# Kernel tuning notes

Hardware: AMD Instinct MI355X
Metric: run time of the kernel (lower is better)

The kernel has to match this reference:

```python
import jax, jax.numpy as jnp
import numpy as np

B, N, DIN, DOUT = 8, 2048, 128, 128

def setup_inputs() -> dict:
    key = jax.random.key(0)
    k1, k2, k3, k4 = jax.random.split(key, 4)
    x = jax.random.normal(k1, (B, N, DIN), dtype=jnp.float32)
    adj = jax.random.uniform(k2, (B, N, N), dtype=jnp.float32)
    W = jax.random.normal(k3, (DIN, DOUT), dtype=jnp.float32) / np.sqrt(DIN)
    b = jax.random.normal(k4, (DOUT,), dtype=jnp.float32) * 0.01
    return {"x": x, "adj": adj, "W": W, "b": b}

def reference(x, adj, W, b):
    # degree over last dim of adj: [B, N]
    degree = jnp.sum(adj, axis=2)
    d_norm = 1.0 / jnp.sqrt(degree + 1e-8)
    # D^{-1/2} A D^{-1/2} == row/col elementwise scaling (same math as diag_embed+bmm)
    adj_norm = d_norm[:, :, None] * adj * d_norm[:, None, :]
    support = jnp.einsum('bnm,bmd->bnd', adj_norm, x)  # [B, N, DIN]
    return support @ W + b  # [B, N, DOUT]
```

## Files before the change

### kernel.cpp

```cpp
#include <hip/hip_runtime.h>
#include <hip/hip_bf16.h>

#define NN 2048
#define DD 128

typedef __attribute__((ext_vector_type(4))) float f32x4;
typedef __attribute__((ext_vector_type(8))) short short8;
typedef __attribute__((ext_vector_type(2))) unsigned int u32x2;

__device__ __forceinline__ unsigned short f2bf_bits(float f) {
  union { __hip_bfloat16 h; unsigned short s; } u;
  u.h = __float2bfloat16(f);
  return u.s;
}

__device__ __forceinline__ short8 cvt8(f32x4 a, f32x4 b) {
  short8 r;
  r[0] = (short)f2bf_bits(a[0]); r[1] = (short)f2bf_bits(a[1]);
  r[2] = (short)f2bf_bits(a[2]); r[3] = (short)f2bf_bits(a[3]);
  r[4] = (short)f2bf_bits(b[0]); r[5] = (short)f2bf_bits(b[1]);
  r[6] = (short)f2bf_bits(b[2]); r[7] = (short)f2bf_bits(b[3]);
  return r;
}

__global__ void k_degree(const float* __restrict__ adj, float* __restrict__ dnorm) {
  const int wv = threadIdx.x >> 6;
  const int ln = threadIdx.x & 63;
  const int row = blockIdx.x * 4 + wv;
  const f32x4* rowp = (const f32x4*)(adj + (size_t)row * NN);
  float s = 0.0f;
#pragma unroll
  for (int i = 0; i < 8; ++i) {
    f32x4 v = rowp[i * 64 + ln];
    s += v[0] + v[1] + v[2] + v[3];
  }
#pragma unroll
  for (int off = 32; off >= 1; off >>= 1) s += __shfl_xor(s, off);
  if (ln == 0) dnorm[row] = rsqrtf(s + 1e-8f);
}

__global__ void k_y(const float* __restrict__ x, const float* __restrict__ W,
                    const float* __restrict__ dnorm, short* __restrict__ yT) {
  const int ln = threadIdx.x & 63;
  const int wv = threadIdx.x >> 6;
  const int bb = blockIdx.x >> 5;
  const int n0 = (blockIdx.x & 31) << 6;
  const int l15 = ln & 15, l4 = ln >> 4;
  const int dbase = wv * 32;

  short8 af[2][4];
#pragma unroll
  for (int dt = 0; dt < 2; ++dt)
#pragma unroll
    for (int ks = 0; ks < 4; ++ks) {
      short8 a;
#pragma unroll
      for (int j = 0; j < 8; ++j)
        a[j] = (short)f2bf_bits(W[(size_t)(ks * 32 + l4 * 8 + j) * DD + dbase + dt * 16 + l15]);
      af[dt][ks] = a;
    }

  f32x4 acc[2][4];
#pragma unroll
  for (int dt = 0; dt < 2; ++dt)
#pragma unroll
    for (int nt = 0; nt < 4; ++nt) acc[dt][nt] = (f32x4)0.0f;

  const float* xb = x + (size_t)bb * NN * DD;
  const float* dnb = dnorm + (size_t)bb * NN;
#pragma unroll
  for (int nt = 0; nt < 4; ++nt) {
    const int n = n0 + nt * 16 + l15;
    const float dn = dnb[n];
#pragma unroll
    for (int ks = 0; ks < 4; ++ks) {
      f32x4 p = *(const f32x4*)(xb + (size_t)n * DD + ks * 32 + l4 * 8);
      f32x4 q = *(const f32x4*)(xb + (size_t)n * DD + ks * 32 + l4 * 8 + 4);
      short8 bf = cvt8(p * dn, q * dn);
#pragma unroll
      for (int dt = 0; dt < 2; ++dt)
        acc[dt][nt] = __builtin_amdgcn_mfma_f32_16x16x32_bf16(af[dt][ks], bf, acc[dt][nt], 0, 0, 0);
    }
  }

  short* yb = yT + (size_t)bb * DD * NN;
#pragma unroll
  for (int dt = 0; dt < 2; ++dt)
#pragma unroll
    for (int nt = 0; nt < 4; ++nt)
#pragma unroll
      for (int r = 0; r < 4; ++r) {
        int d = dbase + dt * 16 + l4 * 4 + r;
        yb[(size_t)d * NN + n0 + nt * 16 + l15] = (short)f2bf_bits(acc[dt][nt][r]);
      }
}

__launch_bounds__(512, 4)
__global__ void k_gemm(const float* __restrict__ adj, const short* __restrict__ yT,
                       const float* __restrict__ dnorm, const float* __restrict__ bias,
                       float* __restrict__ out) {
  __shared__ short As[4][2048];

  const int t = threadIdx.x;
  const int ln = t & 63;
  const int wv = t >> 6;
  const int orig = ((blockIdx.x & 7) << 6) | (blockIdx.x >> 3);
  const int bb = orig >> 6;
  const int m0 = (orig & 63) << 5;

  const float* ablk = adj + ((size_t)bb * NN + m0) * NN;
  const int oc = (wv << 4) + (ln & 15);
  const int kg8 = (ln >> 4) << 3;
  const short* ybase = yT + ((size_t)bb * DD + oc) * NN;

  const unsigned srow = (unsigned)t >> 4;
  const unsigned sc4 = ((unsigned)t & 15u) << 2;

  f32x4 acc[2];
  acc[0] = (f32x4)0.0f; acc[1] = (f32x4)0.0f;

  auto loadA = [&](int tile) -> f32x4 {
    return *(const f32x4*)(ablk + (size_t)srow * NN + ((tile & 31) << 6) + sc4);
  };
  auto loadB = [&](int tile, int ks) -> short8 {
    return *(const short8*)(ybase + ((tile & 31) << 6) + ks * 32 + kg8);
  };
  auto writeA = [&](f32x4 v, int buf) {
    unsigned byte = (srow << 7) + (sc4 << 1);
    byte ^= (srow & 7u) << 4;
    u32x2 u;
    u[0] = (unsigned)f2bf_bits(v[0]) | ((unsigned)f2bf_bits(v[1]) << 16);
    u[1] = (unsigned)f2bf_bits(v[2]) | ((unsigned)f2bf_bits(v[3]) << 16);
    *(u32x2*)((char*)As + (buf << 12) + byte) = u;
  };
  auto compute = [&](int buf, short8 b0, short8 b1) {
    const char* base = (const char*)As + (buf << 12);
#pragma unroll
    for (int ks = 0; ks < 2; ++ks) {
      short8 bf = ks ? b1 : b0;
#pragma unroll
      for (int m = 0; m < 2; ++m) {
        unsigned row = (unsigned)(m * 16 + (ln & 15));
        unsigned byte = (row << 7) + (unsigned)((ks * 32 + kg8) << 1);
        byte ^= (row & 7u) << 4;
        short8 a = *(const short8*)(base + byte);
        acc[m] = __builtin_amdgcn_mfma_f32_16x16x32_bf16(a, bf, acc[m], 0, 0, 0);
      }
    }
  };

  f32x4 sA0 = loadA(0), sA1 = loadA(1), sA2 = loadA(2), sA3 = loadA(3);
  short8 bE0 = loadB(0, 0), bE1 = loadB(0, 1);
  short8 bO0 = loadB(1, 0), bO1 = loadB(1, 1);
  writeA(sA0, 0);
  asm volatile("s_waitcnt lgkmcnt(0)\n\ts_barrier" ::: "memory");

#define GITER(T, SNEW, SWR, BC0, BC1)                                 \
  {                                                                   \
    SNEW = loadA((T) + 4);                                            \
    short8 nb0 = loadB((T) + 2, 0), nb1 = loadB((T) + 2, 1);          \
    writeA(SWR, ((T) + 1) & 3);                                       \
    asm volatile("s_waitcnt lgkmcnt(0)\n\ts_barrier" ::: "memory");   \
    compute((T) & 3, BC0, BC1);                                       \
    BC0 = nb0; BC1 = nb1;                                             \
  }

#pragma unroll 1
  for (int t4 = 0; t4 < 32; t4 += 4) {
    GITER(t4 + 0, sA0, sA1, bE0, bE1);
    GITER(t4 + 1, sA1, sA2, bO0, bO1);
    GITER(t4 + 2, sA2, sA3, bE0, bE1);
    GITER(t4 + 3, sA3, sA0, bO0, bO1);
  }
#undef GITER

  const float bv = bias[oc];
  const int rbase = (ln >> 4) << 2;
#pragma unroll
  for (int m = 0; m < 2; ++m) {
    f32x4 dn = *(const f32x4*)(dnorm + (size_t)bb * NN + m0 + m * 16 + rbase);
#pragma unroll
    for (int r = 0; r < 4; ++r)
      out[(size_t)(bb * NN + m0 + m * 16 + rbase + r) * DD + oc] = acc[m][r] * dn[r] + bv;
  }
}

extern "C" void kernel_launch(void* const* d_in, const int* in_sizes, int n_in,
                              void* d_out, int out_size, void* d_ws, size_t ws_size,
                              hipStream_t stream) {
  (void)in_sizes; (void)n_in; (void)out_size; (void)ws_size;
  const float* x = (const float*)d_in[0];
  const float* adj = (const float*)d_in[1];
  const float* W = (const float*)d_in[2];
  const float* bias = (const float*)d_in[3];
  float* out = (float*)d_out;

  char* ws = (char*)d_ws;
  float* dnorm = (float*)ws;
  short* yT = (short*)(ws + (1 << 16));

  k_degree<<<4096, 256, 0, stream>>>(adj, dnorm);
  k_y<<<256, 256, 0, stream>>>(x, W, dnorm, yT);
  k_gemm<<<512, 512, 0, stream>>>(adj, yT, dnorm, bias, out);
}
```

Measured before the change: 69.25 us.

## Fuse degree, projection and aggregation into one cooperative kernel reading adj once

```diff
diff --git a/kernel.cpp b/kernel.cpp
--- a/kernel.cpp
+++ b/kernel.cpp
@@ -1,8 +1,11 @@
 #include <hip/hip_runtime.h>
 #include <hip/hip_bf16.h>
+#include <hip/hip_cooperative_groups.h>
 
 #define NN 2048
 #define DD 128
+
+namespace cg = cooperative_groups;
 
 typedef __attribute__((ext_vector_type(4))) float f32x4;
 typedef __attribute__((ext_vector_type(8))) short short8;
@@ -21,6 +24,161 @@
   r[4] = (short)f2bf_bits(b[0]); r[5] = (short)f2bf_bits(b[1]);
   r[6] = (short)f2bf_bits(b[2]); r[7] = (short)f2bf_bits(b[3]);
   return r;
+}
+
+__device__ __forceinline__ u32x2 pack4(f32x4 v) {
+  u32x2 u;
+  u[0] = (unsigned)f2bf_bits(v[0]) | ((unsigned)f2bf_bits(v[1]) << 16);
+  u[1] = (unsigned)f2bf_bits(v[2]) | ((unsigned)f2bf_bits(v[3]) << 16);
+  return u;
+}
+
+#define ABIG_S 1032
+#define DBUF_S 72
+__launch_bounds__(512, 2)
+__global__ void k_fused(const float* __restrict__ adj, const float* __restrict__ x,
+                        const float* __restrict__ W, const float* __restrict__ bias,
+                        float* __restrict__ out, short* __restrict__ yT) {
+  __shared__ short Abig[64 * ABIG_S];
+  __shared__ short dbuf[2][64 * DBUF_S];
+  __shared__ float dnl[64];
+
+  const int t = threadIdx.x;
+  const int ln = t & 63;
+  const int wv = t >> 6;
+  const int l15 = ln & 15, l4 = ln >> 4;
+
+  const int orig = ((blockIdx.x & 7) << 5) | (blockIdx.x >> 3);
+  const int bb = orig >> 5;
+  const int rowblk = orig & 31;
+  const size_t rowg0 = (size_t)bb * NN + (rowblk << 6);
+
+  const int r = t >> 3, c8 = t & 7;
+  const float* arow = adj + (rowg0 + r) * NN + (c8 << 2);
+  char* awr = (char*)Abig + r * (ABIG_S * 2) + (c8 << 3);
+
+  float s0 = 0.f, s1 = 0.f;
+  u32x2 areg[32];
+#pragma unroll
+  for (int T = 0; T < 32; ++T) {
+    f32x4 v = *(const f32x4*)(arow + T * 32);
+    s0 += v[0] + v[1]; s1 += v[2] + v[3];
+    *(u32x2*)(awr + T * 64) = pack4(v);
+  }
+#pragma unroll
+  for (int T = 0; T < 32; ++T) {
+    f32x4 v = *(const f32x4*)(arow + (32 + T) * 32);
+    s0 += v[0] + v[1]; s1 += v[2] + v[3];
+    areg[T] = pack4(v);
+  }
+  float s = s0 + s1;
+  s += __shfl_xor(s, 1); s += __shfl_xor(s, 2); s += __shfl_xor(s, 4);
+  if (c8 == 0) dnl[r] = rsqrtf(s + 1e-8f);
+  __syncthreads();
+
+  {
+    const int nch = rowblk << 6;
+    const int dbase = (wv & 3) << 5;
+    const int nh = (wv >> 2) << 5;
+    short8 af[2][4];
+#pragma unroll
+    for (int dt = 0; dt < 2; ++dt)
+#pragma unroll
+      for (int ks = 0; ks < 4; ++ks) {
+        short8 a;
+#pragma unroll
+        for (int j = 0; j < 8; ++j)
+          a[j] = (short)f2bf_bits(W[(size_t)(ks * 32 + l4 * 8 + j) * DD + dbase + dt * 16 + l15]);
+        af[dt][ks] = a;
+      }
+    f32x4 acc2[2][2];
+    acc2[0][0] = (f32x4)0.f; acc2[0][1] = (f32x4)0.f;
+    acc2[1][0] = (f32x4)0.f; acc2[1][1] = (f32x4)0.f;
+#pragma unroll
+    for (int nt = 0; nt < 2; ++nt) {
+      const int nloc = nh + nt * 16 + l15;
+      const float dn = dnl[nloc];
+      const float* xr = x + ((size_t)bb * NN + nch + nloc) * DD;
+#pragma unroll
+      for (int ks = 0; ks < 4; ++ks) {
+        f32x4 p = *(const f32x4*)(xr + ks * 32 + l4 * 8);
+        f32x4 q = *(const f32x4*)(xr + ks * 32 + l4 * 8 + 4);
+        short8 bf = cvt8(p * dn, q * dn);
+        acc2[0][nt] = __builtin_amdgcn_mfma_f32_16x16x32_bf16(af[0][ks], bf, acc2[0][nt], 0, 0, 0);
+        acc2[1][nt] = __builtin_amdgcn_mfma_f32_16x16x32_bf16(af[1][ks], bf, acc2[1][nt], 0, 0, 0);
+      }
+    }
+    short* yb = yT + (size_t)bb * DD * NN;
+#pragma unroll
+    for (int dt = 0; dt < 2; ++dt)
+#pragma unroll
+      for (int nt = 0; nt < 2; ++nt)
+#pragma unroll
+        for (int rr = 0; rr < 4; ++rr)
+          yb[(size_t)(dbase + dt * 16 + l4 * 4 + rr) * NN + nch + nh + nt * 16 + l15] =
+              (short)f2bf_bits(acc2[dt][nt][rr]);
+  }
+
+  cg::this_grid().sync();
+
+  const int oc = (wv << 4) + l15;
+  const int kg8 = l4 << 3;
+  const short* ybase = yT + ((size_t)bb * DD + oc) * NN;
+  char* dwr = (char*)dbuf + r * (DBUF_S * 2) + (c8 << 3);
+
+  f32x4 acc[4];
+#pragma unroll
+  for (int m = 0; m < 4; ++m) acc[m] = (f32x4)0.f;
+
+  auto loadB = [&](int kt, int ks) -> short8 {
+    return *(const short8*)(ybase + (kt << 6) + ks * 32 + kg8);
+  };
+  auto ctile = [&](const char* tb, unsigned rstride, short8 b0, short8 b1) {
+#pragma unroll
+    for (int ks = 0; ks < 2; ++ks) {
+      short8 bf = ks ? b1 : b0;
+#pragma unroll
+      for (int m = 0; m < 4; ++m) {
+        unsigned row = (unsigned)(m * 16 + l15);
+        unsigned byte = row * rstride + (unsigned)((ks * 32 + kg8) << 1);
+        short8 a = *(const short8*)(tb + byte);
+        acc[m] = __builtin_amdgcn_mfma_f32_16x16x32_bf16(a, bf, acc[m], 0, 0, 0);
+      }
+    }
+  };
+
+  *(u32x2*)dwr = areg[0];
+  *(u32x2*)(dwr + 64) = areg[1];
+  short8 bA0 = loadB(0, 0), bA1 = loadB(0, 1);
+  short8 bD0 = loadB(16, 0), bD1 = loadB(16, 1);
+  asm volatile("s_waitcnt lgkmcnt(0)\n\ts_barrier" ::: "memory");
+
+#pragma unroll
+  for (int j = 0; j < 16; ++j) {
+    if (j < 15) {
+      *(u32x2*)(dwr + ((j + 1) & 1) * (64 * DBUF_S * 2)) = areg[2 * j + 2];
+      *(u32x2*)(dwr + ((j + 1) & 1) * (64 * DBUF_S * 2) + 64) = areg[2 * j + 3];
+    }
+    short8 nA0 = bA0, nA1 = bA1, nD0 = bD0, nD1 = bD1;
+    if (j < 15) {
+      nA0 = loadB(j + 1, 0); nA1 = loadB(j + 1, 1);
+      nD0 = loadB(17 + j, 0); nD1 = loadB(17 + j, 1);
+    }
+    ctile((const char*)Abig + j * 128, (unsigned)(ABIG_S * 2), bA0, bA1);
+    ctile((const char*)dbuf + (j & 1) * (64 * DBUF_S * 2), (unsigned)(DBUF_S * 2), bD0, bD1);
+    asm volatile("s_waitcnt lgkmcnt(0)\n\ts_barrier" ::: "memory");
+    bA0 = nA0; bA1 = nA1; bD0 = nD0; bD1 = nD1;
+  }
+
+  const float bv = bias[oc];
+  const int rb = l4 << 2;
+#pragma unroll
+  for (int m = 0; m < 4; ++m)
+#pragma unroll
+    for (int rr = 0; rr < 4; ++rr) {
+      const int row = m * 16 + rb + rr;
+      out[(rowg0 + row) * DD + oc] = acc[m][rr] * dnl[row] + bv;
+    }
 }
 
 __global__ void k_degree(const float* __restrict__ adj, float* __restrict__ dnorm) {
@@ -89,9 +247,9 @@
 #pragma unroll
     for (int nt = 0; nt < 4; ++nt)
 #pragma unroll
-      for (int r = 0; r < 4; ++r) {
-        int d = dbase + dt * 16 + l4 * 4 + r;
-        yb[(size_t)d * NN + n0 + nt * 16 + l15] = (short)f2bf_bits(acc[dt][nt][r]);
+      for (int rr = 0; rr < 4; ++rr) {
+        int d = dbase + dt * 16 + l4 * 4 + rr;
+        yb[(size_t)d * NN + n0 + nt * 16 + l15] = (short)f2bf_bits(acc[dt][nt][rr]);
       }
 }
 
@@ -128,10 +286,7 @@
   auto writeA = [&](f32x4 v, int buf) {
     unsigned byte = (srow << 7) + (sc4 << 1);
     byte ^= (srow & 7u) << 4;
-    u32x2 u;
-    u[0] = (unsigned)f2bf_bits(v[0]) | ((unsigned)f2bf_bits(v[1]) << 16);
-    u[1] = (unsigned)f2bf_bits(v[2]) | ((unsigned)f2bf_bits(v[3]) << 16);
-    *(u32x2*)((char*)As + (buf << 12) + byte) = u;
+    *(u32x2*)((char*)As + (buf << 12) + byte) = pack4(v);
   };
   auto compute = [&](int buf, short8 b0, short8 b1) {
     const char* base = (const char*)As + (buf << 12);
@@ -180,8 +335,8 @@
   for (int m = 0; m < 2; ++m) {
     f32x4 dn = *(const f32x4*)(dnorm + (size_t)bb * NN + m0 + m * 16 + rbase);
 #pragma unroll
-    for (int r = 0; r < 4; ++r)
-      out[(size_t)(bb * NN + m0 + m * 16 + rbase + r) * DD + oc] = acc[m][r] * dn[r] + bv;
+    for (int rr = 0; rr < 4; ++rr)
+      out[(size_t)(bb * NN + m0 + m * 16 + rbase + rr) * DD + oc] = acc[m][rr] * dn[rr] + bv;
   }
 }
 
@@ -199,7 +354,14 @@
   float* dnorm = (float*)ws;
   short* yT = (short*)(ws + (1 << 16));
 
-  k_degree<<<4096, 256, 0, stream>>>(adj, dnorm);
-  k_y<<<256, 256, 0, stream>>>(x, W, dnorm, yT);
-  k_gemm<<<512, 512, 0, stream>>>(adj, yT, dnorm, bias, out);
-}
+  void* args[] = {(void*)&adj, (void*)&x, (void*)&W, (void*)&bias,
+                  (void*)&out, (void*)&yT};
+  hipError_t e = hipLaunchCooperativeKernel((const void*)k_fused, dim3(256),
+                                            dim3(512), args, 0, stream);
+  if (e != hipSuccess) {
+    (void)hipGetLastError();
+    k_degree<<<4096, 256, 0, stream>>>(adj, dnorm);
+    k_y<<<256, 256, 0, stream>>>(x, W, dnorm, yT);
+    k_gemm<<<512, 512, 0, stream>>>(adj, yT, dnorm, bias, out);
+  }
+}
```

Result: slower. 101.2 us (+46.1%).

## Replace LDS-staged GEMM with per-wave direct-register MFMA tiles

Applied to the files above, without the earlier changes.

```diff
diff --git a/kernel.cpp b/kernel.cpp
--- a/kernel.cpp
+++ b/kernel.cpp
@@ -6,7 +6,6 @@
 
 typedef __attribute__((ext_vector_type(4))) float f32x4;
 typedef __attribute__((ext_vector_type(8))) short short8;
-typedef __attribute__((ext_vector_type(2))) unsigned int u32x2;
 
 __device__ __forceinline__ unsigned short f2bf_bits(float f) {
   union { __hip_bfloat16 h; unsigned short s; } u;
@@ -89,99 +88,88 @@
 #pragma unroll
     for (int nt = 0; nt < 4; ++nt)
 #pragma unroll
-      for (int r = 0; r < 4; ++r) {
-        int d = dbase + dt * 16 + l4 * 4 + r;
-        yb[(size_t)d * NN + n0 + nt * 16 + l15] = (short)f2bf_bits(acc[dt][nt][r]);
+      for (int rr = 0; rr < 4; ++rr) {
+        int d = dbase + dt * 16 + l4 * 4 + rr;
+        yb[(size_t)d * NN + n0 + nt * 16 + l15] = (short)f2bf_bits(acc[dt][nt][rr]);
       }
 }
 
-__launch_bounds__(512, 4)
-__global__ void k_gemm(const float* __restrict__ adj, const short* __restrict__ yT,
-                       const float* __restrict__ dnorm, const float* __restrict__ bias,
-                       float* __restrict__ out) {
-  __shared__ short As[4][2048];
-
-  const int t = threadIdx.x;
-  const int ln = t & 63;
-  const int wv = t >> 6;
+__launch_bounds__(256, 2)
+__global__ void k_wgemm(const float* __restrict__ adj, const short* __restrict__ yT,
+                        const float* __restrict__ dnorm, const float* __restrict__ bias,
+                        float* __restrict__ out) {
+  const int ln = threadIdx.x & 63;
+  const int wv = threadIdx.x >> 6;
+  const int l15 = ln & 15, l4 = ln >> 4;
   const int orig = ((blockIdx.x & 7) << 6) | (blockIdx.x >> 3);
   const int bb = orig >> 6;
-  const int m0 = (orig & 63) << 5;
+  const int gw = ((orig & 63) << 2) | wv;
+  const int rowtile = gw >> 1;
+  const int d0 = (gw & 1) << 6;
+  const size_t m0g = (size_t)bb * NN + ((size_t)rowtile << 4);
 
-  const float* ablk = adj + ((size_t)bb * NN + m0) * NN;
-  const int oc = (wv << 4) + (ln & 15);
-  const int kg8 = (ln >> 4) << 3;
-  const short* ybase = yT + ((size_t)bb * DD + oc) * NN;
+  const float* arow = adj + (m0g + l15) * NN + (l4 << 3);
+  const short* ybb = yT + (size_t)bb * DD * NN + (l4 << 3);
+  const short* br0 = ybb + (size_t)(d0 + l15) * NN;
+  const short* br1 = ybb + (size_t)(d0 + 16 + l15) * NN;
+  const short* br2 = ybb + (size_t)(d0 + 32 + l15) * NN;
+  const short* br3 = ybb + (size_t)(d0 + 48 + l15) * NN;
 
-  const unsigned srow = (unsigned)t >> 4;
-  const unsigned sc4 = ((unsigned)t & 15u) << 2;
+  f32x4 acc0 = (f32x4)0.f, acc1 = (f32x4)0.f, acc2 = (f32x4)0.f, acc3 = (f32x4)0.f;
 
-  f32x4 acc[2];
-  acc[0] = (f32x4)0.0f; acc[1] = (f32x4)0.0f;
+  f32x4 a0L = *(const f32x4*)(arow + 0 * 32), a0H = *(const f32x4*)(arow + 0 * 32 + 4);
+  f32x4 a1L = *(const f32x4*)(arow + 1 * 32), a1H = *(const f32x4*)(arow + 1 * 32 + 4);
+  f32x4 a2L = *(const f32x4*)(arow + 2 * 32), a2H = *(const f32x4*)(arow + 2 * 32 + 4);
+  f32x4 a3L = *(const f32x4*)(arow + 3 * 32), a3H = *(const f32x4*)(arow + 3 * 32 + 4);
+  short8 e0 = *(const short8*)(br0 + 0), e1 = *(const short8*)(br1 + 0);
+  short8 e2 = *(const short8*)(br2 + 0), e3 = *(const short8*)(br3 + 0);
+  short8 o0 = *(const short8*)(br0 + 32), o1 = *(const short8*)(br1 + 32);
+  short8 o2 = *(const short8*)(br2 + 32), o3 = *(const short8*)(br3 + 32);
 
-  auto loadA = [&](int tile) -> f32x4 {
-    return *(const f32x4*)(ablk + (size_t)srow * NN + ((tile & 31) << 6) + sc4);
-  };
-  auto loadB = [&](int tile, int ks) -> short8 {
-    return *(const short8*)(ybase + ((tile & 31) << 6) + ks * 32 + kg8);
-  };
-  auto writeA = [&](f32x4 v, int buf) {
-    unsigned byte = (srow << 7) + (sc4 << 1);
-    byte ^= (srow & 7u) << 4;
-    u32x2 u;
-    u[0] = (unsigned)f2bf_bits(v[0]) | ((unsigned)f2bf_bits(v[1]) << 16);
-    u[1] = (unsigned)f2bf_bits(v[2]) | ((unsigned)f2bf_bits(v[3]) << 16);
-    *(u32x2*)((char*)As + (buf << 12) + byte) = u;
-  };
-  auto compute = [&](int buf, short8 b0, short8 b1) {
-    const char* base = (const char*)As + (buf << 12);
-#pragma unroll
-    for (int ks = 0; ks < 2; ++ks) {
-      short8 bf = ks ? b1 : b0;
-#pragma unroll
-      for (int m = 0; m < 2; ++m) {
-        unsigned row = (unsigned)(m * 16 + (ln & 15));
-        unsigned byte = (row << 7) + (unsigned)((ks * 32 + kg8) << 1);
-        byte ^= (row & 7u) << 4;
-        short8 a = *(const short8*)(base + byte);
-        acc[m] = __builtin_amdgcn_mfma_f32_16x16x32_bf16(a, bf, acc[m], 0, 0, 0);
-      }
-    }
-  };
-
-  f32x4 sA0 = loadA(0), sA1 = loadA(1), sA2 = loadA(2), sA3 = loadA(3);
-  short8 bE0 = loadB(0, 0), bE1 = loadB(0, 1);
-  short8 bO0 = loadB(1, 0), bO1 = loadB(1, 1);
-  writeA(sA0, 0);
-  asm volatile("s_waitcnt lgkmcnt(0)\n\ts_barrier" ::: "memory");
-
-#define GITER(T, SNEW, SWR, BC0, BC1)                                 \
-  {                                                                   \
-    SNEW = loadA((T) + 4);                                            \
-    short8 nb0 = loadB((T) + 2, 0), nb1 = loadB((T) + 2, 1);          \
-    writeA(SWR, ((T) + 1) & 3);                                       \
-    asm volatile("s_waitcnt lgkmcnt(0)\n\ts_barrier" ::: "memory");   \
-    compute((T) & 3, BC0, BC1);                                       \
-    BC0 = nb0; BC1 = nb1;                                             \
+#define KS(J, AL, AH, B0_, B1_, B2_, B3_, DOA, DOB)                          \
+  {                                                                          \
+    short8 af = cvt8(AL, AH);                                                \
+    acc0 = __builtin_amdgcn_mfma_f32_16x16x32_bf16(af, B0_, acc0, 0, 0, 0);  \
+    acc1 = __builtin_amdgcn_mfma_f32_16x16x32_bf16(af, B1_, acc1, 0, 0, 0);  \
+    acc2 = __builtin_amdgcn_mfma_f32_16x16x32_bf16(af, B2_, acc2, 0, 0, 0);  \
+    acc3 = __builtin_amdgcn_mfma_f32_16x16x32_bf16(af, B3_, acc3, 0, 0, 0);  \
+    if (DOA) {                                                               \
+      AL = *(const f32x4*)(arow + ((J) + 4) * 32);                           \
+      AH = *(const f32x4*)(arow + ((J) + 4) * 32 + 4);                       \
+    }                                                                        \
+    if (DOB) {                                                               \
+      B0_ = *(const short8*)(br0 + ((J) + 2) * 32);                          \
+      B1_ = *(const short8*)(br1 + ((J) + 2) * 32);                          \
+      B2_ = *(const short8*)(br2 + ((J) + 2) * 32);                          \
+      B3_ = *(const short8*)(br3 + ((J) + 2) * 32);                          \
+    }                                                                        \
   }
 
 #pragma unroll 1
-  for (int t4 = 0; t4 < 32; t4 += 4) {
-    GITER(t4 + 0, sA0, sA1, bE0, bE1);
-    GITER(t4 + 1, sA1, sA2, bO0, bO1);
-    GITER(t4 + 2, sA2, sA3, bE0, bE1);
-    GITER(t4 + 3, sA3, sA0, bO0, bO1);
+  for (int j = 0; j < 60; j += 4) {
+    KS(j + 0, a0L, a0H, e0, e1, e2, e3, 1, 1);
+    KS(j + 1, a1L, a1H, o0, o1, o2, o3, 1, 1);
+    KS(j + 2, a2L, a2H, e0, e1, e2, e3, 1, 1);
+    KS(j + 3, a3L, a3H, o0, o1, o2, o3, 1, 1);
   }
-#undef GITER
+  KS(60, a0L, a0H, e0, e1, e2, e3, 0, 1);
+  KS(61, a1L, a1H, o0, o1, o2, o3, 0, 1);
+  KS(62, a2L, a2H, e0, e1, e2, e3, 0, 0);
+  KS(63, a3L, a3H, o0, o1, o2, o3, 0, 0);
+#undef KS
 
-  const float bv = bias[oc];
-  const int rbase = (ln >> 4) << 2;
+  f32x4 dn4 = *(const f32x4*)(dnorm + m0g + (l4 << 2));
+  const float bv0 = bias[d0 + l15];
+  const float bv1 = bias[d0 + 16 + l15];
+  const float bv2 = bias[d0 + 32 + l15];
+  const float bv3 = bias[d0 + 48 + l15];
 #pragma unroll
-  for (int m = 0; m < 2; ++m) {
-    f32x4 dn = *(const f32x4*)(dnorm + (size_t)bb * NN + m0 + m * 16 + rbase);
-#pragma unroll
-    for (int r = 0; r < 4; ++r)
-      out[(size_t)(bb * NN + m0 + m * 16 + rbase + r) * DD + oc] = acc[m][r] * dn[r] + bv;
+  for (int rr = 0; rr < 4; ++rr) {
+    const size_t base = (m0g + (l4 << 2) + rr) * DD + d0 + l15;
+    out[base] = acc0[rr] * dn4[rr] + bv0;
+    out[base + 16] = acc1[rr] * dn4[rr] + bv1;
+    out[base + 32] = acc2[rr] * dn4[rr] + bv2;
+    out[base + 48] = acc3[rr] * dn4[rr] + bv3;
   }
 }
 
@@ -201,5 +189,5 @@
 
   k_degree<<<4096, 256, 0, stream>>>(adj, dnorm);
   k_y<<<256, 256, 0, stream>>>(x, W, dnorm, yT);
-  k_gemm<<<512, 512, 0, stream>>>(adj, yT, dnorm, bias, out);
+  k_wgemm<<<512, 256, 0, stream>>>(adj, yT, dnorm, bias, out);
 }
```

After: 118.8 us. 71.6% more time.

## Retile adjacency GEMM to 16-row blocks with 4 waves covering 32 columns each

Applied to the files above, without the earlier changes.

```diff
diff --git a/kernel.cpp b/kernel.cpp
--- a/kernel.cpp
+++ b/kernel.cpp
@@ -21,6 +21,13 @@
   r[4] = (short)f2bf_bits(b[0]); r[5] = (short)f2bf_bits(b[1]);
   r[6] = (short)f2bf_bits(b[2]); r[7] = (short)f2bf_bits(b[3]);
   return r;
+}
+
+__device__ __forceinline__ u32x2 pack4(f32x4 v) {
+  u32x2 u;
+  u[0] = (unsigned)f2bf_bits(v[0]) | ((unsigned)f2bf_bits(v[1]) << 16);
+  u[1] = (unsigned)f2bf_bits(v[2]) | ((unsigned)f2bf_bits(v[3]) << 16);
+  return u;
 }
 
 __global__ void k_degree(const float* __restrict__ adj, float* __restrict__ dnorm) {
@@ -89,99 +96,96 @@
 #pragma unroll
     for (int nt = 0; nt < 4; ++nt)
 #pragma unroll
-      for (int r = 0; r < 4; ++r) {
-        int d = dbase + dt * 16 + l4 * 4 + r;
-        yb[(size_t)d * NN + n0 + nt * 16 + l15] = (short)f2bf_bits(acc[dt][nt][r]);
+      for (int rr = 0; rr < 4; ++rr) {
+        int d = dbase + dt * 16 + l4 * 4 + rr;
+        yb[(size_t)d * NN + n0 + nt * 16 + l15] = (short)f2bf_bits(acc[dt][nt][rr]);
       }
 }
 
-__launch_bounds__(512, 4)
-__global__ void k_gemm(const float* __restrict__ adj, const short* __restrict__ yT,
-                       const float* __restrict__ dnorm, const float* __restrict__ bias,
-                       float* __restrict__ out) {
-  __shared__ short As[4][2048];
+__launch_bounds__(256, 4)
+__global__ void k_gemm16(const float* __restrict__ adj, const short* __restrict__ yT,
+                         const float* __restrict__ dnorm, const float* __restrict__ bias,
+                         float* __restrict__ out) {
+  __shared__ short As[4][1024];
 
   const int t = threadIdx.x;
   const int ln = t & 63;
   const int wv = t >> 6;
-  const int orig = ((blockIdx.x & 7) << 6) | (blockIdx.x >> 3);
-  const int bb = orig >> 6;
-  const int m0 = (orig & 63) << 5;
-
-  const float* ablk = adj + ((size_t)bb * NN + m0) * NN;
-  const int oc = (wv << 4) + (ln & 15);
-  const int kg8 = (ln >> 4) << 3;
-  const short* ybase = yT + ((size_t)bb * DD + oc) * NN;
-
-  const unsigned srow = (unsigned)t >> 4;
-  const unsigned sc4 = ((unsigned)t & 15u) << 2;
-
-  f32x4 acc[2];
-  acc[0] = (f32x4)0.0f; acc[1] = (f32x4)0.0f;
-
-  auto loadA = [&](int tile) -> f32x4 {
-    return *(const f32x4*)(ablk + (size_t)srow * NN + ((tile & 31) << 6) + sc4);
-  };
-  auto loadB = [&](int tile, int ks) -> short8 {
-    return *(const short8*)(ybase + ((tile & 31) << 6) + ks * 32 + kg8);
+  const int l15 = ln & 15, l4 = ln >> 4;
+  const int orig = ((blockIdx.x & 7) << 7) | (blockIdx.x >> 3);
+  const int bb = orig >> 7;
+  const int m0 = (orig & 127) << 4;
+  const size_t m0g = (size_t)bb * NN + m0;
+
+  const float* ablk = adj + m0g * NN;
+  const int dbase = wv << 5;
+  const short* yb0 = yT + ((size_t)bb * DD + dbase + l15) * NN + (l4 << 3);
+  const short* yb1 = yT + ((size_t)bb * DD + dbase + 16 + l15) * NN + (l4 << 3);
+
+  const int srow = t >> 4;
+  const int sc4 = (t & 15) << 2;
+
+  f32x4 acc0 = (f32x4)0.f, acc1 = (f32x4)0.f;
+
+  auto loadA = [&](int kt) -> f32x4 {
+    return *(const f32x4*)(ablk + (size_t)srow * NN + (kt << 6) + sc4);
   };
   auto writeA = [&](f32x4 v, int buf) {
-    unsigned byte = (srow << 7) + (sc4 << 1);
-    byte ^= (srow & 7u) << 4;
-    u32x2 u;
-    u[0] = (unsigned)f2bf_bits(v[0]) | ((unsigned)f2bf_bits(v[1]) << 16);
-    u[1] = (unsigned)f2bf_bits(v[2]) | ((unsigned)f2bf_bits(v[3]) << 16);
-    *(u32x2*)((char*)As + (buf << 12) + byte) = u;
+    unsigned byte = ((unsigned)srow << 7) + ((unsigned)sc4 << 1);
+    byte ^= ((unsigned)srow & 7u) << 4;
+    *(u32x2*)((char*)As + (buf << 11) + byte) = pack4(v);
   };
-  auto compute = [&](int buf, short8 b0, short8 b1) {
-    const char* base = (const char*)As + (buf << 12);
-#pragma unroll
-    for (int ks = 0; ks < 2; ++ks) {
-      short8 bf = ks ? b1 : b0;
-#pragma unroll
-      for (int m = 0; m < 2; ++m) {
-        unsigned row = (unsigned)(m * 16 + (ln & 15));
-        unsigned byte = (row << 7) + (unsigned)((ks * 32 + kg8) << 1);
-        byte ^= (row & 7u) << 4;
-        short8 a = *(const short8*)(base + byte);
-        acc[m] = __builtin_amdgcn_mfma_f32_16x16x32_bf16(a, bf, acc[m], 0, 0, 0);
-      }
-    }
+  auto compute = [&](int buf, short8 b00, short8 b01, short8 b10, short8 b11) {
+    const char* base = (const char*)As + (buf << 11);
+    unsigned b0 = ((unsigned)l15 << 7) + ((unsigned)l4 << 4);
+    unsigned sw = ((unsigned)l15 & 7u) << 4;
+    short8 a0 = *(const short8*)(base + (b0 ^ sw));
+    short8 a1 = *(const short8*)(base + ((b0 + 64) ^ sw));
+    acc0 = __builtin_amdgcn_mfma_f32_16x16x32_bf16(a0, b00, acc0, 0, 0, 0);
+    acc0 = __builtin_amdgcn_mfma_f32_16x16x32_bf16(a1, b01, acc0, 0, 0, 0);
+    acc1 = __builtin_amdgcn_mfma_f32_16x16x32_bf16(a0, b10, acc1, 0, 0, 0);
+    acc1 = __builtin_amdgcn_mfma_f32_16x16x32_bf16(a1, b11, acc1, 0, 0, 0);
   };
 
-  f32x4 sA0 = loadA(0), sA1 = loadA(1), sA2 = loadA(2), sA3 = loadA(3);
-  short8 bE0 = loadB(0, 0), bE1 = loadB(0, 1);
-  short8 bO0 = loadB(1, 0), bO1 = loadB(1, 1);
-  writeA(sA0, 0);
+  f32x4 s0 = loadA(0), s1 = loadA(1), s2 = loadA(2), s3 = loadA(3);
+  short8 c00 = *(const short8*)(yb0 + 0), c01 = *(const short8*)(yb0 + 32);
+  short8 c10 = *(const short8*)(yb1 + 0), c11 = *(const short8*)(yb1 + 32);
+  writeA(s0, 0);
   asm volatile("s_waitcnt lgkmcnt(0)\n\ts_barrier" ::: "memory");
 
-#define GITER(T, SNEW, SWR, BC0, BC1)                                 \
-  {                                                                   \
-    SNEW = loadA((T) + 4);                                            \
-    short8 nb0 = loadB((T) + 2, 0), nb1 = loadB((T) + 2, 1);          \
-    writeA(SWR, ((T) + 1) & 3);                                       \
-    asm volatile("s_waitcnt lgkmcnt(0)\n\ts_barrier" ::: "memory");   \
-    compute((T) & 3, BC0, BC1);                                       \
-    BC0 = nb0; BC1 = nb1;                                             \
+#define GITER(T, SNEW, SWR)                                             \
+  {                                                                     \
+    if ((T) < 28) SNEW = loadA((T) + 4);                                \
+    short8 n00 = c00, n01 = c01, n10 = c10, n11 = c11;                  \
+    if ((T) < 31) {                                                     \
+      n00 = *(const short8*)(yb0 + ((T) + 1) * 64);                     \
+      n01 = *(const short8*)(yb0 + ((T) + 1) * 64 + 32);                \
+      n10 = *(const short8*)(yb1 + ((T) + 1) * 64);                     \
+      n11 = *(const short8*)(yb1 + ((T) + 1) * 64 + 32);                \
+      writeA(SWR, ((T) + 1) & 3);                                       \
+    }                                                                   \
+    asm volatile("s_waitcnt lgkmcnt(0)\n\ts_barrier" ::: "memory");     \
+    compute((T) & 3, c00, c01, c10, c11);                               \
+    c00 = n00; c01 = n01; c10 = n10; c11 = n11;                         \
   }
 
 #pragma unroll 1
   for (int t4 = 0; t4 < 32; t4 += 4) {
-    GITER(t4 + 0, sA0, sA1, bE0, bE1);
-    GITER(t4 + 1, sA1, sA2, bO0, bO1);
-    GITER(t4 + 2, sA2, sA3, bE0, bE1);
-    GITER(t4 + 3, sA3, sA0, bO0, bO1);
+    GITER(t4 + 0, s0, s1);
+    GITER(t4 + 1, s1, s2);
+    GITER(t4 + 2, s2, s3);
+    GITER(t4 + 3, s3, s0);
   }
 #undef GITER
 
-  const float bv = bias[oc];
-  const int rbase = (ln >> 4) << 2;
-#pragma unroll
-  for (int m = 0; m < 2; ++m) {
-    f32x4 dn = *(const f32x4*)(dnorm + (size_t)bb * NN + m0 + m * 16 + rbase);
-#pragma unroll
-    for (int r = 0; r < 4; ++r)
-      out[(size_t)(bb * NN + m0 + m * 16 + rbase + r) * DD + oc] = acc[m][r] * dn[r] + bv;
+  f32x4 dn4 = *(const f32x4*)(dnorm + m0g + (l4 << 2));
+  const float bv0 = bias[dbase + l15];
+  const float bv1 = bias[dbase + 16 + l15];
+#pragma unroll
+  for (int rr = 0; rr < 4; ++rr) {
+    const size_t base = (m0g + (l4 << 2) + rr) * DD + dbase + l15;
+    out[base] = acc0[rr] * dn4[rr] + bv0;
+    out[base + 16] = acc1[rr] * dn4[rr] + bv1;
   }
 }
 
@@ -201,5 +205,5 @@
 
   k_degree<<<4096, 256, 0, stream>>>(adj, dnorm);
   k_y<<<256, 256, 0, stream>>>(x, W, dnorm, yT);
-  k_gemm<<<512, 512, 0, stream>>>(adj, yT, dnorm, bias, out);
-}
+  k_gemm16<<<1024, 256, 0, stream>>>(adj, yT, dnorm, bias, out);
+}
```

After: 95.50 us. 1.38x slower.
